# Kernel optimization log

Hardware: AMD Instinct MI355X
Metric: run time of the kernel (lower is better)

## Reference

```python
import jax, jax.numpy as jnp
import numpy as np

B, C, V = 4096, 1000, 8000   # batch, NUM_COMPO, NUM_CHARS
THRESH = 0.8                 # compo_score_thresh
SCALE = 0.1                  # score_adjustment_scale
TOPK = 5


def setup_inputs() -> dict:
    key = jax.random.key(0)
    k1, k2, k3, k4 = jax.random.split(key, 4)
    return {
        "pred_class_logits": jax.random.normal(k1, (B, V), jnp.float32),
        "pred_compo_logits": jax.random.normal(k2, (B, C), jnp.float32),
        "compo_co_occurrence_prob": jax.random.uniform(k3, (C, C), dtype=jnp.float32),
        "compo_chinese_matrix": jax.random.randint(k4, (C, V), 0, 2, dtype=jnp.int32),
    }


def _decode_one(compo_scores, co_occ, matrix):
    """components_to_chinese_char for one sample. compo_scores:[C], co_occ:[C,C], matrix:[C,V]."""
    nC, nV = matrix.shape
    # score adjustment from co-occurrence of components above threshold
    sel = compo_scores > THRESH                                   # [C]
    adj = SCALE * jnp.sum(
        jnp.where(sel[:, None], co_occ * compo_scores[:, None], 0.0), axis=0)  # [C]
    scores = compo_scores + adj
    max_idx = jnp.argmax(scores)
    max_score = scores[max_idx]
    # re-threshold and sort selected scores descending (fixed-shape: mask with -inf)
    sel2 = scores > THRESH
    num_selected = jnp.sum(sel2.astype(jnp.int32))
    masked = jnp.where(sel2, scores, -jnp.inf)
    order = jnp.argsort(-masked)          # descending; selected compo indices first
    sorted_scores = masked[order]
    hit0 = matrix[max_idx]                # [V] 0/1

    def cond(carry):
        i, hit, _ = carry
        return (i < num_selected) & (jnp.sum(hit) > 1)

    def body(carry):
        i, hit, _ = carry
        row = matrix[order[i]]
        new_hit = jnp.where(hit + row == 2, 1, 0).astype(jnp.int32)  # intersection
        return (i + 1, new_hit, hit)

    i0 = jnp.array(1, jnp.int32)
    i, hit, prev = jax.lax.while_loop(cond, body, (i0, hit0, hit0))
    empty = jnp.sum(hit) == 0
    i = jnp.where(empty, i - 1, i)
    hit = jnp.where(empty, prev, hit)
    hit_score = jnp.where(i == 1, max_score, sorted_scores[jnp.maximum(i - 1, 0)])
    # first 5 hit char indices (ascending, as tf.where yields), padded with -1
    char_ids = jnp.where(hit == 1, jnp.arange(nV), nV)
    first5 = jnp.sort(char_ids)[:TOPK]
    hit_indices = jnp.where(first5 == nV, -1, first5).astype(jnp.int32)
    return hit_indices, hit_score


def reference(pred_class_logits, pred_compo_logits, compo_co_occurrence_prob, compo_chinese_matrix):
    class_probs = jax.nn.softmax(pred_class_logits, axis=1)            # [B,V]
    class_scores, class_indices = jax.lax.top_k(class_probs, TOPK)     # [B,5]
    compo_scores = jax.nn.sigmoid(pred_compo_logits)                   # [B,C]
    hit_indices, hit_scores = jax.vmap(_decode_one, in_axes=(0, None, None))(
        compo_scores, compo_co_occurrence_prob, compo_chinese_matrix)
    class_indices = class_indices.astype(jnp.int32)
    num_hit = jnp.sum((hit_indices != -1).astype(jnp.int32), axis=1)   # [B]
    combined1 = jnp.where(num_hit == 1, hit_indices[:, 0], class_indices[:, 0])
    combined2 = jnp.where((class_scores[:, 0] < 0.85) & (num_hit == 1),
                          hit_indices[:, 0], class_indices[:, 0])
    return (class_indices, class_scores, hit_indices, hit_scores, combined1, combined2)
```

## Files before the change

### kernel.cpp

```cpp
#include <hip/hip_runtime.h>
#include <cstdint>
#include <cstddef>

#define B_SZ 4096
#define C_SZ 1000
#define V_SZ 8000
#define RW 128
#define THRESHF 0.8f
#define SCALEF 0.1f

#define OFF_CI 0
#define OFF_CS (B_SZ * 5)
#define OFF_HI (2 * B_SZ * 5)
#define OFF_HS (3 * B_SZ * 5)
#define OFF_C1 (3 * B_SZ * 5 + B_SZ)
#define OFF_C2 (3 * B_SZ * 5 + 2 * B_SZ)

__global__ __launch_bounds__(256) void pack_kernel(const int* __restrict__ mat,
                                                   unsigned long long* __restrict__ packed) {
  const int c = blockIdx.x;
  const int tid = threadIdx.x;
  const int lane = tid & 63;
  const int wv = tid >> 6;
  const int* row = mat + (size_t)c * V_SZ;
  for (int base = 0; base < 8192; base += 256) {
    const int k = base + tid;
    int v = 0;
    if (k < V_SZ) v = row[k];
    unsigned long long msk = __ballot(v != 0);
    if (lane == 0) packed[(size_t)c * RW + ((base >> 6) + wv)] = msk;
  }
}

__global__ __launch_bounds__(256) void class_topk_kernel(const float* __restrict__ logits,
                                                         float* __restrict__ out) {
  const int b = blockIdx.x;
  const int tid = threadIdx.x;
  const int lane = tid & 63;
  const int wv = tid >> 6;
  const float* row = logits + (size_t)b * V_SZ;
  float v[32];
#pragma unroll
  for (int q = 0; q < 32; ++q) {
    int k = tid + (q << 8);
    v[q] = (k < V_SZ) ? row[k] : -INFINITY;
  }
  __shared__ float sred[4];
  __shared__ int sredi[4];
  float lm = -INFINITY;
#pragma unroll
  for (int q = 0; q < 32; ++q) lm = fmaxf(lm, v[q]);
#pragma unroll
  for (int o = 32; o >= 1; o >>= 1) lm = fmaxf(lm, __shfl_xor(lm, o));
  if (lane == 0) sred[wv] = lm;
  __syncthreads();
  const float m = fmaxf(fmaxf(sred[0], sred[1]), fmaxf(sred[2], sred[3]));
  float ls = 0.f;
#pragma unroll
  for (int q = 0; q < 32; ++q) ls += expf(v[q] - m);
#pragma unroll
  for (int o = 32; o >= 1; o >>= 1) ls += __shfl_xor(ls, o);
  __syncthreads();
  if (lane == 0) sred[wv] = ls;
  __syncthreads();
  const float ssum = sred[0] + sred[1] + sred[2] + sred[3];
  for (int r = 0; r < 5; ++r) {
    float bv = -INFINITY;
    int bi = 0;
#pragma unroll
    for (int q = 0; q < 32; ++q) {
      if (v[q] > bv) { bv = v[q]; bi = tid + (q << 8); }
    }
#pragma unroll
    for (int o = 32; o >= 1; o >>= 1) {
      float ov = __shfl_xor(bv, o);
      int oi = __shfl_xor(bi, o);
      if (ov > bv || (ov == bv && oi < bi)) { bv = ov; bi = oi; }
    }
    __syncthreads();
    if (lane == 0) { sred[wv] = bv; sredi[wv] = bi; }
    __syncthreads();
    bv = sred[0]; bi = sredi[0];
#pragma unroll
    for (int w = 1; w < 4; ++w) {
      if (sred[w] > bv || (sred[w] == bv && sredi[w] < bi)) { bv = sred[w]; bi = sredi[w]; }
    }
    if ((bi & 255) == tid) {
      const int sl = bi >> 8;
#pragma unroll
      for (int q = 0; q < 32; ++q)
        if (q == sl) v[q] = -INFINITY;
    }
    if (tid == 0) {
      out[OFF_CI + b * 5 + r] = (float)bi;
      out[OFF_CS + b * 5 + r] = expf(bv - m) / ssum;
    }
  }
}

__global__ __launch_bounds__(256) void decode_kernel(const float* __restrict__ compo_logits,
                                                     const float* __restrict__ co_occ,
                                                     const unsigned long long* __restrict__ packed,
                                                     float* __restrict__ out) {
  const int b = blockIdx.x;
  const int tid = threadIdx.x;
  const int lane = tid & 63;
  const int wv = tid >> 6;
  __shared__ float s_m[C_SZ];
  __shared__ float s_sc[1024];
  __shared__ short s_list[C_SZ];
  __shared__ int s_nsel;
  __shared__ float red_v[4];
  __shared__ int red_i[4];
  __shared__ int red_n[4];

  const float* lg = compo_logits + (size_t)b * C_SZ;
  for (int k = tid; k < 1024; k += 256) {
    if (k < C_SZ) {
      float x = lg[k];
      float s = 1.0f / (1.0f + expf(-x));
      s_sc[k] = s;
      s_m[k] = (s > THRESHF) ? s : 0.0f;
    } else {
      s_sc[k] = -INFINITY;
    }
  }
  __syncthreads();
  if (wv == 0) {
    int off = 0;
    for (int base = 0; base < C_SZ; base += 64) {
      const int k = base + lane;
      float mv = (k < C_SZ) ? s_m[k] : 0.0f;
      unsigned long long msk = __ballot(mv != 0.0f);
      int rank = __popcll(msk & ((1ull << lane) - 1ull));
      if (mv != 0.0f) s_list[off + rank] = (short)k;
      off += __popcll(msk);
    }
    if (lane == 0) s_nsel = off;
  }
  __syncthreads();
  const int nadj = s_nsel;
  float a0 = 0.f, a1 = 0.f, a2 = 0.f, a3 = 0.f;
  for (int e = 0; e < nadj; ++e) {
    const int i = s_list[e];
    const float mm = s_m[i];
    const float* rp = co_occ + (size_t)i * C_SZ;
    a0 += mm * rp[tid];
    a1 += mm * rp[tid + 256];
    a2 += mm * rp[tid + 512];
    if (tid < C_SZ - 768) a3 += mm * rp[tid + 768];
  }
  float bv = -INFINITY;
  int bi = 0;
  int cnt = 0;
  {
    float sc;
    sc = s_sc[tid] + SCALEF * a0;
    s_sc[tid] = sc;
    if (sc > THRESHF) cnt++;
    if (sc > bv) { bv = sc; bi = tid; }
    sc = s_sc[tid + 256] + SCALEF * a1;
    s_sc[tid + 256] = sc;
    if (sc > THRESHF) cnt++;
    if (sc > bv) { bv = sc; bi = tid + 256; }
    sc = s_sc[tid + 512] + SCALEF * a2;
    s_sc[tid + 512] = sc;
    if (sc > THRESHF) cnt++;
    if (sc > bv) { bv = sc; bi = tid + 512; }
    if (tid < C_SZ - 768) {
      sc = s_sc[tid + 768] + SCALEF * a3;
      s_sc[tid + 768] = sc;
      if (sc > THRESHF) cnt++;
      if (sc > bv) { bv = sc; bi = tid + 768; }
    }
  }
#pragma unroll
  for (int o = 32; o >= 1; o >>= 1) {
    float ov = __shfl_xor(bv, o);
    int oi = __shfl_xor(bi, o);
    cnt += __shfl_xor(cnt, o);
    if (ov > bv || (ov == bv && oi < bi)) { bv = ov; bi = oi; }
  }
  if (lane == 0) { red_v[wv] = bv; red_i[wv] = bi; red_n[wv] = cnt; }
  __syncthreads();
  float mxv = red_v[0];
  int mxi = red_i[0];
  const int nsel = red_n[0] + red_n[1] + red_n[2] + red_n[3];
#pragma unroll
  for (int w = 1; w < 4; ++w) {
    if (red_v[w] > mxv || (red_v[w] == mxv && red_i[w] < mxi)) { mxv = red_v[w]; mxi = red_i[w]; }
  }
  if (tid == 0) s_sc[mxi] = -INFINITY;
  __syncthreads();
  if (wv != 0) return;

  float p[16];
#pragma unroll
  for (int q = 0; q < 16; ++q) {
    const int k = lane + (q << 6);
    p[q] = (k < C_SZ) ? s_sc[k] : -INFINITY;
  }
  const unsigned long long* pr = packed + (size_t)mxi * RW;
  unsigned long long h0 = pr[lane];
  unsigned long long h1 = pr[64 + lane];
  int pc = __popcll(h0) + __popcll(h1);
#pragma unroll
  for (int o = 32; o >= 1; o >>= 1) pc += __shfl_xor(pc, o);
  int i = 1;
  float last_v = mxv;
  unsigned long long ph0 = h0, ph1 = h1;
  int ppc = pc;
  float plast = mxv;
  while (i < nsel && pc > 1) {
    float ev = -INFINITY;
    int ei = 0;
#pragma unroll
    for (int q = 0; q < 16; ++q) {
      if (p[q] > ev) { ev = p[q]; ei = lane + (q << 6); }
    }
#pragma unroll
    for (int o = 32; o >= 1; o >>= 1) {
      float ov = __shfl_xor(ev, o);
      int oi = __shfl_xor(ei, o);
      if (ov > ev || (ov == ev && oi < ei)) { ev = ov; ei = oi; }
    }
    if ((ei & 63) == lane) {
      const int sl = ei >> 6;
#pragma unroll
      for (int q = 0; q < 16; ++q)
        if (q == sl) p[q] = -INFINITY;
    }
    const unsigned long long* r2 = packed + (size_t)ei * RW;
    ph0 = h0; ph1 = h1; ppc = pc; plast = last_v;
    h0 &= r2[lane];
    h1 &= r2[64 + lane];
    pc = __popcll(h0) + __popcll(h1);
#pragma unroll
    for (int o = 32; o >= 1; o >>= 1) pc += __shfl_xor(pc, o);
    last_v = ev;
    ++i;
  }
  if (pc == 0) {
    h0 = ph0; h1 = ph1; pc = ppc; last_v = plast;
  }
  const float hit_score = last_v;

  const int c0 = __popcll(h0), c1 = __popcll(h1);
  int s0 = c0;
#pragma unroll
  for (int o = 1; o < 64; o <<= 1) {
    int n = __shfl_up(s0, o);
    if (lane >= o) s0 += n;
  }
  const int tot0 = __shfl(s0, 63);
  const int pre0 = s0 - c0;
  int s1 = c1;
#pragma unroll
  for (int o = 1; o < 64; o <<= 1) {
    int n = __shfl_up(s1, o);
    if (lane >= o) s1 += n;
  }
  const int tot = tot0 + __shfl(s1, 63);
  const int pre1 = tot0 + s1 - c1;
  {
    unsigned long long x = h0;
    int r = pre0;
    while (x && r < 5) {
      int bp = __ffsll((unsigned long long)x) - 1;
      out[OFF_HI + b * 5 + r] = (float)((lane << 6) + bp);
      x &= x - 1;
      ++r;
    }
    x = h1;
    r = pre1;
    while (x && r < 5) {
      int bp = __ffsll((unsigned long long)x) - 1;
      out[OFF_HI + b * 5 + r] = (float)(((64 + lane) << 6) + bp);
      x &= x - 1;
      ++r;
    }
  }
  int fb = 0x7fffffff;
  if (c0) fb = (lane << 6) + __ffsll((unsigned long long)h0) - 1;
  else if (c1) fb = ((64 + lane) << 6) + __ffsll((unsigned long long)h1) - 1;
#pragma unroll
  for (int o = 32; o >= 1; o >>= 1) fb = min(fb, __shfl_xor(fb, o));
  if (lane == 0) {
    const int num_hit = tot < 5 ? tot : 5;
    for (int r = num_hit; r < 5; ++r) out[OFF_HI + b * 5 + r] = -1.0f;
    out[OFF_HS + b] = hit_score;
    const float ci0 = out[OFF_CI + b * 5];
    const float cs0 = out[OFF_CS + b * 5];
    out[OFF_C1 + b] = (num_hit == 1) ? (float)fb : ci0;
    out[OFF_C2 + b] = (cs0 < 0.85f && num_hit == 1) ? (float)fb : ci0;
  }
}

extern "C" void kernel_launch(void* const* d_in, const int* in_sizes, int n_in,
                              void* d_out, int out_size, void* d_ws, size_t ws_size,
                              hipStream_t stream) {
  (void)in_sizes; (void)n_in; (void)out_size; (void)ws_size;
  const float* class_logits = (const float*)d_in[0];
  const float* compo_logits = (const float*)d_in[1];
  const float* co_occ = (const float*)d_in[2];
  const int* mat = (const int*)d_in[3];
  float* out = (float*)d_out;
  unsigned long long* packed = (unsigned long long*)d_ws;

  pack_kernel<<<C_SZ, 256, 0, stream>>>(mat, packed);
  class_topk_kernel<<<B_SZ, 256, 0, stream>>>(class_logits, out);
  decode_kernel<<<B_SZ, 256, 0, stream>>>(compo_logits, co_occ, packed, out);
}
```

Measured before the change: 156.7 us.

## Batch sorted intersection across all four waves with shared-memory row staging

Rewrites the decode kernel's sequential greedy intersection. Before, one wave pulled one next-best component per iteration and did a dependent global load each time. Now all four waves select their local top-16 candidates, a merge step picks a global batch of 16, their packed rows are staged into LDS cooperatively, and running popcounts find the stop point inside the batch. It also switches the co-occurrence adjustment and the sigmoid load to float4 vectorised access, unrolled over four selected rows. The cost is more synchronisation per batch and extra LDS, which can lower occupancy, plus complex tie and stop handling that could diverge from the reference in edge cases.

```diff
diff --git a/kernel.cpp b/kernel.cpp
--- a/kernel.cpp
+++ b/kernel.cpp
@@ -1,6 +1,8 @@
 #include <hip/hip_runtime.h>
 #include <cstdint>
 #include <cstddef>
+
+typedef unsigned long long u64;
 
 #define B_SZ 4096
 #define C_SZ 1000
@@ -17,7 +19,7 @@
 #define OFF_C2 (3 * B_SZ * 5 + 2 * B_SZ)
 
 __global__ __launch_bounds__(256) void pack_kernel(const int* __restrict__ mat,
-                                                   unsigned long long* __restrict__ packed) {
+                                                   u64* __restrict__ packed) {
   const int c = blockIdx.x;
   const int tid = threadIdx.x;
   const int lane = tid & 63;
@@ -27,7 +29,7 @@
     const int k = base + tid;
     int v = 0;
     if (k < V_SZ) v = row[k];
-    unsigned long long msk = __ballot(v != 0);
+    u64 msk = __ballot(v != 0);
     if (lane == 0) packed[(size_t)c * RW + ((base >> 6) + wv)] = msk;
   }
 }
@@ -100,79 +102,102 @@
 
 __global__ __launch_bounds__(256) void decode_kernel(const float* __restrict__ compo_logits,
                                                      const float* __restrict__ co_occ,
-                                                     const unsigned long long* __restrict__ packed,
+                                                     const u64* __restrict__ packed,
                                                      float* __restrict__ out) {
   const int b = blockIdx.x;
   const int tid = threadIdx.x;
   const int lane = tid & 63;
   const int wv = tid >> 6;
-  __shared__ float s_m[C_SZ];
+
   __shared__ float s_sc[1024];
-  __shared__ short s_list[C_SZ];
-  __shared__ int s_nsel;
+  __shared__ int s_list[C_SZ];
+  __shared__ u64 s_rows[16][128];
+  __shared__ float s_wv_v[4][16];
+  __shared__ int s_wv_i[4][16];
+  __shared__ float s_gv[16];
+  __shared__ int s_gi[16];
   __shared__ float red_v[4];
   __shared__ int red_i[4];
   __shared__ int red_n[4];
+  __shared__ int s_nsel2;
+  __shared__ int s_mxi;
+  __shared__ float s_mxv;
+  __shared__ int s_nadj;
+  __shared__ int s_ctl;
 
   const float* lg = compo_logits + (size_t)b * C_SZ;
-  for (int k = tid; k < 1024; k += 256) {
-    if (k < C_SZ) {
-      float x = lg[k];
-      float s = 1.0f / (1.0f + expf(-x));
-      s_sc[k] = s;
-      s_m[k] = (s > THRESHF) ? s : 0.0f;
-    } else {
-      s_sc[k] = -INFINITY;
-    }
-  }
-  __syncthreads();
+  if (tid < 250) {
+    float4 x = ((const float4*)lg)[tid];
+    s_sc[4 * tid + 0] = 1.0f / (1.0f + expf(-x.x));
+    s_sc[4 * tid + 1] = 1.0f / (1.0f + expf(-x.y));
+    s_sc[4 * tid + 2] = 1.0f / (1.0f + expf(-x.z));
+    s_sc[4 * tid + 3] = 1.0f / (1.0f + expf(-x.w));
+  } else {
+    s_sc[4 * tid + 0] = -INFINITY;
+    s_sc[4 * tid + 1] = -INFINITY;
+    s_sc[4 * tid + 2] = -INFINITY;
+    s_sc[4 * tid + 3] = -INFINITY;
+  }
+  __syncthreads();
+
   if (wv == 0) {
     int off = 0;
     for (int base = 0; base < C_SZ; base += 64) {
       const int k = base + lane;
-      float mv = (k < C_SZ) ? s_m[k] : 0.0f;
-      unsigned long long msk = __ballot(mv != 0.0f);
+      float mv = (k < C_SZ) ? s_sc[k] : -INFINITY;
+      bool sel = (k < C_SZ) && (mv > THRESHF);
+      u64 msk = __ballot(sel);
       int rank = __popcll(msk & ((1ull << lane) - 1ull));
-      if (mv != 0.0f) s_list[off + rank] = (short)k;
+      if (sel) s_list[off + rank] = k;
       off += __popcll(msk);
     }
-    if (lane == 0) s_nsel = off;
-  }
-  __syncthreads();
-  const int nadj = s_nsel;
+    if (lane == 0) s_nadj = off;
+  }
+  __syncthreads();
+  const int nadj = s_nadj;
+
   float a0 = 0.f, a1 = 0.f, a2 = 0.f, a3 = 0.f;
-  for (int e = 0; e < nadj; ++e) {
-    const int i = s_list[e];
-    const float mm = s_m[i];
-    const float* rp = co_occ + (size_t)i * C_SZ;
-    a0 += mm * rp[tid];
-    a1 += mm * rp[tid + 256];
-    a2 += mm * rp[tid + 512];
-    if (tid < C_SZ - 768) a3 += mm * rp[tid + 768];
-  }
+  if (tid < 250) {
+    const float4* cov = (const float4*)co_occ;
+    int e = 0;
+    for (; e + 4 <= nadj; e += 4) {
+      int i0 = s_list[e], i1 = s_list[e + 1], i2 = s_list[e + 2], i3 = s_list[e + 3];
+      float m0 = s_sc[i0], m1 = s_sc[i1], m2 = s_sc[i2], m3 = s_sc[i3];
+      float4 v0 = cov[i0 * 250 + tid];
+      float4 v1 = cov[i1 * 250 + tid];
+      float4 v2 = cov[i2 * 250 + tid];
+      float4 v3 = cov[i3 * 250 + tid];
+      a0 += m0 * v0.x; a0 += m1 * v1.x; a0 += m2 * v2.x; a0 += m3 * v3.x;
+      a1 += m0 * v0.y; a1 += m1 * v1.y; a1 += m2 * v2.y; a1 += m3 * v3.y;
+      a2 += m0 * v0.z; a2 += m1 * v1.z; a2 += m2 * v2.z; a2 += m3 * v3.z;
+      a3 += m0 * v0.w; a3 += m1 * v1.w; a3 += m2 * v2.w; a3 += m3 * v3.w;
+    }
+    for (; e < nadj; ++e) {
+      int i = s_list[e];
+      float m = s_sc[i];
+      float4 v = cov[i * 250 + tid];
+      a0 += m * v.x; a1 += m * v.y; a2 += m * v.z; a3 += m * v.w;
+    }
+  }
+  __syncthreads();
+
   float bv = -INFINITY;
   int bi = 0;
   int cnt = 0;
-  {
+  if (tid < 250) {
     float sc;
-    sc = s_sc[tid] + SCALEF * a0;
-    s_sc[tid] = sc;
+    sc = s_sc[4 * tid + 0] + SCALEF * a0; s_sc[4 * tid + 0] = sc;
     if (sc > THRESHF) cnt++;
-    if (sc > bv) { bv = sc; bi = tid; }
-    sc = s_sc[tid + 256] + SCALEF * a1;
-    s_sc[tid + 256] = sc;
+    if (sc > bv) { bv = sc; bi = 4 * tid + 0; }
+    sc = s_sc[4 * tid + 1] + SCALEF * a1; s_sc[4 * tid + 1] = sc;
     if (sc > THRESHF) cnt++;
-    if (sc > bv) { bv = sc; bi = tid + 256; }
-    sc = s_sc[tid + 512] + SCALEF * a2;
-    s_sc[tid + 512] = sc;
+    if (sc > bv) { bv = sc; bi = 4 * tid + 1; }
+    sc = s_sc[4 * tid + 2] + SCALEF * a2; s_sc[4 * tid + 2] = sc;
     if (sc > THRESHF) cnt++;
-    if (sc > bv) { bv = sc; bi = tid + 512; }
-    if (tid < C_SZ - 768) {
-      sc = s_sc[tid + 768] + SCALEF * a3;
-      s_sc[tid + 768] = sc;
-      if (sc > THRESHF) cnt++;
-      if (sc > bv) { bv = sc; bi = tid + 768; }
-    }
+    if (sc > bv) { bv = sc; bi = 4 * tid + 2; }
+    sc = s_sc[4 * tid + 3] + SCALEF * a3; s_sc[4 * tid + 3] = sc;
+    if (sc > THRESHF) cnt++;
+    if (sc > bv) { bv = sc; bi = 4 * tid + 3; }
   }
 #pragma unroll
   for (int o = 32; o >= 1; o >>= 1) {
@@ -183,116 +208,211 @@
   }
   if (lane == 0) { red_v[wv] = bv; red_i[wv] = bi; red_n[wv] = cnt; }
   __syncthreads();
-  float mxv = red_v[0];
-  int mxi = red_i[0];
-  const int nsel = red_n[0] + red_n[1] + red_n[2] + red_n[3];
-#pragma unroll
-  for (int w = 1; w < 4; ++w) {
-    if (red_v[w] > mxv || (red_v[w] == mxv && red_i[w] < mxi)) { mxv = red_v[w]; mxi = red_i[w]; }
-  }
-  if (tid == 0) s_sc[mxi] = -INFINITY;
-  __syncthreads();
-  if (wv != 0) return;
-
-  float p[16];
-#pragma unroll
-  for (int q = 0; q < 16; ++q) {
-    const int k = lane + (q << 6);
-    p[q] = (k < C_SZ) ? s_sc[k] : -INFINITY;
-  }
-  const unsigned long long* pr = packed + (size_t)mxi * RW;
-  unsigned long long h0 = pr[lane];
-  unsigned long long h1 = pr[64 + lane];
-  int pc = __popcll(h0) + __popcll(h1);
-#pragma unroll
-  for (int o = 32; o >= 1; o >>= 1) pc += __shfl_xor(pc, o);
-  int i = 1;
-  float last_v = mxv;
-  unsigned long long ph0 = h0, ph1 = h1;
-  int ppc = pc;
-  float plast = mxv;
-  while (i < nsel && pc > 1) {
-    float ev = -INFINITY;
-    int ei = 0;
-#pragma unroll
-    for (int q = 0; q < 16; ++q) {
-      if (p[q] > ev) { ev = p[q]; ei = lane + (q << 6); }
-    }
-#pragma unroll
-    for (int o = 32; o >= 1; o >>= 1) {
-      float ov = __shfl_xor(ev, o);
-      int oi = __shfl_xor(ei, o);
-      if (ov > ev || (ov == ev && oi < ei)) { ev = ov; ei = oi; }
-    }
-    if ((ei & 63) == lane) {
-      const int sl = ei >> 6;
-#pragma unroll
-      for (int q = 0; q < 16; ++q)
-        if (q == sl) p[q] = -INFINITY;
-    }
-    const unsigned long long* r2 = packed + (size_t)ei * RW;
-    ph0 = h0; ph1 = h1; ppc = pc; plast = last_v;
-    h0 &= r2[lane];
-    h1 &= r2[64 + lane];
-    pc = __popcll(h0) + __popcll(h1);
-#pragma unroll
-    for (int o = 32; o >= 1; o >>= 1) pc += __shfl_xor(pc, o);
-    last_v = ev;
-    ++i;
-  }
-  if (pc == 0) {
-    h0 = ph0; h1 = ph1; pc = ppc; last_v = plast;
-  }
-  const float hit_score = last_v;
-
-  const int c0 = __popcll(h0), c1 = __popcll(h1);
-  int s0 = c0;
-#pragma unroll
-  for (int o = 1; o < 64; o <<= 1) {
-    int n = __shfl_up(s0, o);
-    if (lane >= o) s0 += n;
-  }
-  const int tot0 = __shfl(s0, 63);
-  const int pre0 = s0 - c0;
-  int s1 = c1;
-#pragma unroll
-  for (int o = 1; o < 64; o <<= 1) {
-    int n = __shfl_up(s1, o);
-    if (lane >= o) s1 += n;
-  }
-  const int tot = tot0 + __shfl(s1, 63);
-  const int pre1 = tot0 + s1 - c1;
-  {
-    unsigned long long x = h0;
-    int r = pre0;
-    while (x && r < 5) {
-      int bp = __ffsll((unsigned long long)x) - 1;
-      out[OFF_HI + b * 5 + r] = (float)((lane << 6) + bp);
-      x &= x - 1;
-      ++r;
-    }
-    x = h1;
-    r = pre1;
-    while (x && r < 5) {
-      int bp = __ffsll((unsigned long long)x) - 1;
-      out[OFF_HI + b * 5 + r] = (float)(((64 + lane) << 6) + bp);
-      x &= x - 1;
-      ++r;
-    }
-  }
-  int fb = 0x7fffffff;
-  if (c0) fb = (lane << 6) + __ffsll((unsigned long long)h0) - 1;
-  else if (c1) fb = ((64 + lane) << 6) + __ffsll((unsigned long long)h1) - 1;
-#pragma unroll
-  for (int o = 32; o >= 1; o >>= 1) fb = min(fb, __shfl_xor(fb, o));
-  if (lane == 0) {
-    const int num_hit = tot < 5 ? tot : 5;
-    for (int r = num_hit; r < 5; ++r) out[OFF_HI + b * 5 + r] = -1.0f;
-    out[OFF_HS + b] = hit_score;
-    const float ci0 = out[OFF_CI + b * 5];
-    const float cs0 = out[OFF_CS + b * 5];
-    out[OFF_C1 + b] = (num_hit == 1) ? (float)fb : ci0;
-    out[OFF_C2 + b] = (cs0 < 0.85f && num_hit == 1) ? (float)fb : ci0;
+  if (tid == 0) {
+    float mv = red_v[0];
+    int mi = red_i[0];
+    for (int w = 1; w < 4; ++w)
+      if (red_v[w] > mv || (red_v[w] == mv && red_i[w] < mi)) { mv = red_v[w]; mi = red_i[w]; }
+    s_mxv = mv; s_mxi = mi;
+    s_nsel2 = red_n[0] + red_n[1] + red_n[2] + red_n[3];
+  }
+  __syncthreads();
+  const float mxv = s_mxv;
+  const int mxi = s_mxi;
+  const int nsel = s_nsel2;
+
+  const int ebase = wv << 8;
+  float r0 = s_sc[ebase + lane];
+  float r1 = s_sc[ebase + lane + 64];
+  float r2 = s_sc[ebase + lane + 128];
+  float r3 = s_sc[ebase + lane + 192];
+
+  u64 acc0 = ~0ull, acc1 = ~0ull;
+  float prev_last = mxv;
+  float hitscore = mxv;
+
+  for (int batch = 0; batch < 64; ++batch) {
+    {
+      int rd = 0;
+      for (; rd < 16; ++rd) {
+        float ev = r0;
+        int ei = ebase + lane;
+        if (r1 > ev) { ev = r1; ei = ebase + lane + 64; }
+        if (r2 > ev) { ev = r2; ei = ebase + lane + 128; }
+        if (r3 > ev) { ev = r3; ei = ebase + lane + 192; }
+#pragma unroll
+        for (int o = 32; o >= 1; o >>= 1) {
+          float ov = __shfl_xor(ev, o);
+          int oi = __shfl_xor(ei, o);
+          if (ov > ev || (ov == ev && oi < ei)) { ev = ov; ei = oi; }
+        }
+        if (!(ev > THRESHF)) break;
+        if (lane == 0) { s_wv_v[wv][rd] = ev; s_wv_i[wv][rd] = ei; }
+        int d = ei - ebase;
+        if ((d & 63) == lane) {
+          if (d < 64) r0 = -INFINITY;
+          else if (d < 128) r1 = -INFINITY;
+          else if (d < 192) r2 = -INFINITY;
+          else r3 = -INFINITY;
+        }
+      }
+      if (lane == 0)
+        for (; rd < 16; ++rd) s_wv_v[wv][rd] = -INFINITY;
+    }
+    __syncthreads();
+    if (wv == 0) {
+      float cv = s_wv_v[lane >> 4][lane & 15];
+      int ci = s_wv_i[lane >> 4][lane & 15];
+      int rd = 0;
+      for (; rd < 16; ++rd) {
+        float ev = cv;
+        int ei = ci;
+#pragma unroll
+        for (int o = 32; o >= 1; o >>= 1) {
+          float ov = __shfl_xor(ev, o);
+          int oi = __shfl_xor(ei, o);
+          if (ov > ev || (ov == ev && oi < ei)) { ev = ov; ei = oi; }
+        }
+        if (!(ev > THRESHF)) break;
+        if (lane == 0) { s_gi[rd] = ei; s_gv[rd] = ev; }
+        if (ci == ei) cv = -INFINITY;
+      }
+      if (lane == 0) {
+        for (; rd < 16; ++rd) s_gi[rd] = -1;
+        if (nsel == 0 && batch == 0) { s_gi[0] = mxi; s_gv[0] = mxv; }
+      }
+    }
+    __syncthreads();
+    for (int j = 0; j < 16; ++j) {
+      float val = s_wv_v[wv][j];
+      if (val == -INFINITY) break;
+      int idx = s_wv_i[wv][j];
+      bool consumed = false;
+#pragma unroll
+      for (int k = 0; k < 16; ++k) consumed |= (s_gi[k] == idx);
+      if (!consumed) {
+        int d = idx - ebase;
+        if ((d & 63) == lane) {
+          if (d < 64) r0 = val;
+          else if (d < 128) r1 = val;
+          else if (d < 192) r2 = val;
+          else r3 = val;
+        }
+      }
+    }
+    {
+      int k = tid >> 4;
+      int g = s_gi[k];
+      if (g >= 0) {
+        const u64* src = packed + (size_t)g * RW + ((tid & 15) << 3);
+        u64* dst = &s_rows[k][(tid & 15) << 3];
+#pragma unroll
+        for (int w = 0; w < 8; ++w) dst[w] = src[w];
+      }
+    }
+    __syncthreads();
+    if (wv == 0) {
+      u64 bal = __ballot(lane < 16 && s_gi[lane] >= 0);
+      int take = __popcll(bal);
+      u64 na0 = acc0, na1 = acc1;
+      u64 pk0 = 0, pk1 = 0, pk2 = 0, pk3 = 0;
+      for (int k = 0; k < take; ++k) {
+        na0 &= s_rows[k][lane];
+        na1 &= s_rows[k][64 + lane];
+        u64 pc = (u64)(__popcll(na0) + __popcll(na1));
+        int sh = (k & 3) << 4;
+        if (k < 4) pk0 |= pc << sh;
+        else if (k < 8) pk1 |= pc << sh;
+        else if (k < 12) pk2 |= pc << sh;
+        else pk3 |= pc << sh;
+      }
+#pragma unroll
+      for (int o = 32; o >= 1; o >>= 1) {
+        pk0 += __shfl_xor(pk0, o);
+        pk1 += __shfl_xor(pk1, o);
+        pk2 += __shfl_xor(pk2, o);
+        pk3 += __shfl_xor(pk3, o);
+      }
+      int kstar = -1;
+      unsigned pcs = 0;
+      for (int k = 0; k < take; ++k) {
+        int sh = (k & 3) << 4;
+        u64 w = (k < 4) ? pk0 : ((k < 8) ? pk1 : ((k < 12) ? pk2 : pk3));
+        unsigned pcv = (unsigned)((w >> sh) & 0xffffull);
+        if (pcv <= 1u) { kstar = k; pcs = pcv; break; }
+      }
+      int stop, kfin;
+      if (take == 0) { stop = 1; kfin = 0; hitscore = prev_last; }
+      else if (kstar >= 0) {
+        if (pcs == 0) {
+          stop = 1;
+          if (kstar == 0) { kfin = 0; hitscore = prev_last; }
+          else { kfin = kstar; hitscore = s_gv[kstar - 1]; }
+        } else { stop = 1; kfin = kstar + 1; hitscore = s_gv[kstar]; }
+      } else if (take < 16) { stop = 1; kfin = take; hitscore = s_gv[take - 1]; }
+      else { stop = 0; kfin = 16; }
+      for (int k = 0; k < kfin; ++k) {
+        acc0 &= s_rows[k][lane];
+        acc1 &= s_rows[k][64 + lane];
+      }
+      if (!stop) prev_last = s_gv[15];
+      if (lane == 0) s_ctl = stop;
+    }
+    __syncthreads();
+    if (s_ctl) break;
+  }
+
+  if (wv == 0) {
+    u64 h0 = acc0, h1 = acc1;
+    const int c0 = __popcll(h0), c1 = __popcll(h1);
+    int sc0 = c0;
+#pragma unroll
+    for (int o = 1; o < 64; o <<= 1) {
+      int n = __shfl_up(sc0, o);
+      if (lane >= o) sc0 += n;
+    }
+    const int tot0 = __shfl(sc0, 63);
+    const int pre0 = sc0 - c0;
+    int sc1 = c1;
+#pragma unroll
+    for (int o = 1; o < 64; o <<= 1) {
+      int n = __shfl_up(sc1, o);
+      if (lane >= o) sc1 += n;
+    }
+    const int tot = tot0 + __shfl(sc1, 63);
+    const int pre1 = tot0 + sc1 - c1;
+    {
+      u64 x = h0;
+      int r = pre0;
+      while (x && r < 5) {
+        int bp = __ffsll((unsigned long long)x) - 1;
+        out[OFF_HI + b * 5 + r] = (float)((lane << 6) + bp);
+        x &= x - 1;
+        ++r;
+      }
+      x = h1;
+      r = pre1;
+      while (x && r < 5) {
+        int bp = __ffsll((unsigned long long)x) - 1;
+        out[OFF_HI + b * 5 + r] = (float)(((64 + lane) << 6) + bp);
+        x &= x - 1;
+        ++r;
+      }
+    }
+    int fb = 0x7fffffff;
+    if (c0) fb = (lane << 6) + __ffsll((unsigned long long)h0) - 1;
+    else if (c1) fb = ((64 + lane) << 6) + __ffsll((unsigned long long)h1) - 1;
+#pragma unroll
+    for (int o = 32; o >= 1; o >>= 1) fb = min(fb, __shfl_xor(fb, o));
+    if (lane == 0) {
+      const int num_hit = tot < 5 ? tot : 5;
+      for (int r = num_hit; r < 5; ++r) out[OFF_HI + b * 5 + r] = -1.0f;
+      out[OFF_HS + b] = hitscore;
+      const float ci0 = out[OFF_CI + b * 5];
+      const float cs0 = out[OFF_CS + b * 5];
+      out[OFF_C1 + b] = (num_hit == 1) ? (float)fb : ci0;
+      out[OFF_C2 + b] = (cs0 < 0.85f && num_hit == 1) ? (float)fb : ci0;
+    }
   }
 }
 
@@ -305,7 +425,7 @@
   const float* co_occ = (const float*)d_in[2];
   const int* mat = (const int*)d_in[3];
   float* out = (float*)d_out;
-  unsigned long long* packed = (unsigned long long*)d_ws;
+  u64* packed = (u64*)d_ws;
 
   pack_kernel<<<C_SZ, 256, 0, stream>>>(mat, packed);
   class_topk_kernel<<<B_SZ, 256, 0, stream>>>(class_logits, out);
```

Result: slower. 246.3 us (+57.1%).

## Split decode into batched co-occurrence matvec and wave-per-sample speculative intersection tail

Applied to the files above, without the earlier changes.

Replaces the per-sample decode kernel with two kernels. The first computes the co-occurrence score adjustment for 8 samples per block, so each co_occ row loaded with float4 is shared across samples, and writes the adjusted scores to workspace. The second runs one wavefront per sample, using packed 64-bit value/index keys and intersecting up to 8 candidate rows speculatively per step to shorten the serial while loop. The class top-k load is also vectorized to float4, at the cost of an extra workspace round trip and a fourth launch.

```diff
diff --git a/kernel.cpp b/kernel.cpp
--- a/kernel.cpp
+++ b/kernel.cpp
@@ -1,6 +1,8 @@
 #include <hip/hip_runtime.h>
 #include <cstdint>
 #include <cstddef>
+
+typedef unsigned long long u64;
 
 #define B_SZ 4096
 #define C_SZ 1000
@@ -8,6 +10,7 @@
 #define RW 128
 #define THRESHF 0.8f
 #define SCALEF 0.1f
+#define S_MV 8
 
 #define OFF_CI 0
 #define OFF_CS (B_SZ * 5)
@@ -17,7 +20,7 @@
 #define OFF_C2 (3 * B_SZ * 5 + 2 * B_SZ)
 
 __global__ __launch_bounds__(256) void pack_kernel(const int* __restrict__ mat,
-                                                   unsigned long long* __restrict__ packed) {
+                                                   u64* __restrict__ packed) {
   const int c = blockIdx.x;
   const int tid = threadIdx.x;
   const int lane = tid & 63;
@@ -27,7 +30,7 @@
     const int k = base + tid;
     int v = 0;
     if (k < V_SZ) v = row[k];
-    unsigned long long msk = __ballot(v != 0);
+    u64 msk = __ballot(v != 0);
     if (lane == 0) packed[(size_t)c * RW + ((base >> 6) + wv)] = msk;
   }
 }
@@ -41,9 +44,15 @@
   const float* row = logits + (size_t)b * V_SZ;
   float v[32];
 #pragma unroll
-  for (int q = 0; q < 32; ++q) {
-    int k = tid + (q << 8);
-    v[q] = (k < V_SZ) ? row[k] : -INFINITY;
+  for (int f = 0; f < 8; ++f) {
+    const int base = (f << 10) + (tid << 2);
+    if (base < V_SZ) {
+      float4 x = *(const float4*)(row + base);
+      v[4 * f + 0] = x.x; v[4 * f + 1] = x.y; v[4 * f + 2] = x.z; v[4 * f + 3] = x.w;
+    } else {
+      v[4 * f + 0] = -INFINITY; v[4 * f + 1] = -INFINITY;
+      v[4 * f + 2] = -INFINITY; v[4 * f + 3] = -INFINITY;
+    }
   }
   __shared__ float sred[4];
   __shared__ int sredi[4];
@@ -69,7 +78,8 @@
     int bi = 0;
 #pragma unroll
     for (int q = 0; q < 32; ++q) {
-      if (v[q] > bv) { bv = v[q]; bi = tid + (q << 8); }
+      const int idx = ((q >> 2) << 10) + (tid << 2) + (q & 3);
+      if (v[q] > bv) { bv = v[q]; bi = idx; }
     }
 #pragma unroll
     for (int o = 32; o >= 1; o >>= 1) {
@@ -85,8 +95,8 @@
     for (int w = 1; w < 4; ++w) {
       if (sred[w] > bv || (sred[w] == bv && sredi[w] < bi)) { bv = sred[w]; bi = sredi[w]; }
     }
-    if ((bi & 255) == tid) {
-      const int sl = bi >> 8;
+    if (((bi & 1023) >> 2) == tid) {
+      const int sl = ((bi >> 10) << 2) | (bi & 3);
 #pragma unroll
       for (int q = 0; q < 32; ++q)
         if (q == sl) v[q] = -INFINITY;
@@ -98,175 +108,218 @@
   }
 }
 
-__global__ __launch_bounds__(256) void decode_kernel(const float* __restrict__ compo_logits,
+__global__ __launch_bounds__(256) void matvec_kernel(const float* __restrict__ compo_logits,
                                                      const float* __restrict__ co_occ,
-                                                     const unsigned long long* __restrict__ packed,
-                                                     float* __restrict__ out) {
-  const int b = blockIdx.x;
+                                                     float* __restrict__ sc_arr) {
+  const int b0 = blockIdx.x * S_MV;
   const int tid = threadIdx.x;
   const int lane = tid & 63;
-  const int wv = tid >> 6;
-  __shared__ float s_m[C_SZ];
-  __shared__ float s_sc[1024];
-  __shared__ short s_list[C_SZ];
-  __shared__ int s_nsel;
-  __shared__ float red_v[4];
-  __shared__ int red_i[4];
-  __shared__ int red_n[4];
-
-  const float* lg = compo_logits + (size_t)b * C_SZ;
-  for (int k = tid; k < 1024; k += 256) {
-    if (k < C_SZ) {
-      float x = lg[k];
-      float s = 1.0f / (1.0f + expf(-x));
-      s_sc[k] = s;
-      s_m[k] = (s > THRESHF) ? s : 0.0f;
-    } else {
-      s_sc[k] = -INFINITY;
-    }
-  }
-  __syncthreads();
-  if (wv == 0) {
-    int off = 0;
-    for (int base = 0; base < C_SZ; base += 64) {
-      const int k = base + lane;
-      float mv = (k < C_SZ) ? s_m[k] : 0.0f;
-      unsigned long long msk = __ballot(mv != 0.0f);
-      int rank = __popcll(msk & ((1ull << lane) - 1ull));
-      if (mv != 0.0f) s_list[off + rank] = (short)k;
-      off += __popcll(msk);
-    }
-    if (lane == 0) s_nsel = off;
-  }
-  __syncthreads();
-  const int nadj = s_nsel;
-  float a0 = 0.f, a1 = 0.f, a2 = 0.f, a3 = 0.f;
-  for (int e = 0; e < nadj; ++e) {
-    const int i = s_list[e];
-    const float mm = s_m[i];
-    const float* rp = co_occ + (size_t)i * C_SZ;
-    a0 += mm * rp[tid];
-    a1 += mm * rp[tid + 256];
-    a2 += mm * rp[tid + 512];
-    if (tid < C_SZ - 768) a3 += mm * rp[tid + 768];
-  }
-  float bv = -INFINITY;
-  int bi = 0;
+  const int w = tid >> 6;
+  __shared__ float s_sc[S_MV][C_SZ];
+  __shared__ unsigned s_bm[C_SZ];
+
+  for (int idx = tid; idx < S_MV * 250; idx += 256) {
+    const int sp = idx / 250;
+    const int f = idx - sp * 250;
+    float4 x = ((const float4*)(compo_logits + (size_t)(b0 + sp) * C_SZ))[f];
+    s_sc[sp][4 * f + 0] = 1.0f / (1.0f + expf(-x.x));
+    s_sc[sp][4 * f + 1] = 1.0f / (1.0f + expf(-x.y));
+    s_sc[sp][4 * f + 2] = 1.0f / (1.0f + expf(-x.z));
+    s_sc[sp][4 * f + 3] = 1.0f / (1.0f + expf(-x.w));
+  }
+  __syncthreads();
+  for (int i = tid; i < C_SZ; i += 256) {
+    unsigned mk = 0;
+#pragma unroll
+    for (int sp = 0; sp < S_MV; ++sp) mk |= (s_sc[sp][i] > THRESHF ? 1u : 0u) << sp;
+    s_bm[i] = mk;
+  }
+  __syncthreads();
+  float acc[2][16];
+#pragma unroll
+  for (int s = 0; s < 2; ++s)
+#pragma unroll
+    for (int j = 0; j < 16; ++j) acc[s][j] = 0.0f;
+  const int cb = lane << 4;
+  const unsigned wsel = 0x11u << w;
+  for (int i = 0; i < C_SZ; ++i) {
+    const unsigned bmv = s_bm[i];
+    if (!(bmv & wsel)) continue;
+    float cv[16];
+#pragma unroll
+    for (int f = 0; f < 4; ++f) {
+      const int base = cb + 4 * f;
+      if (base < C_SZ) {
+        float4 x = *(const float4*)(co_occ + (size_t)i * C_SZ + base);
+        cv[4 * f + 0] = x.x; cv[4 * f + 1] = x.y; cv[4 * f + 2] = x.z; cv[4 * f + 3] = x.w;
+      } else {
+        cv[4 * f + 0] = 0.f; cv[4 * f + 1] = 0.f; cv[4 * f + 2] = 0.f; cv[4 * f + 3] = 0.f;
+      }
+    }
+#pragma unroll
+    for (int spl = 0; spl < 2; ++spl) {
+      const int sp = w + 4 * spl;
+      if (bmv & (1u << sp)) {
+        const float ms = s_sc[sp][i];
+#pragma unroll
+        for (int j = 0; j < 16; ++j) acc[spl][j] += ms * cv[j];
+      }
+    }
+  }
+#pragma unroll
+  for (int spl = 0; spl < 2; ++spl) {
+    const int sp = w + 4 * spl;
+    float* dst = sc_arr + (size_t)(b0 + sp) * C_SZ;
+#pragma unroll
+    for (int f = 0; f < 4; ++f) {
+      const int base = cb + 4 * f;
+      if (base < C_SZ) {
+        float4 o;
+        o.x = s_sc[sp][base + 0] + SCALEF * acc[spl][4 * f + 0];
+        o.y = s_sc[sp][base + 1] + SCALEF * acc[spl][4 * f + 1];
+        o.z = s_sc[sp][base + 2] + SCALEF * acc[spl][4 * f + 2];
+        o.w = s_sc[sp][base + 3] + SCALEF * acc[spl][4 * f + 3];
+        *(float4*)(dst + base) = o;
+      }
+    }
+  }
+}
+
+__global__ __launch_bounds__(256) void tail_kernel(const float* __restrict__ sc_arr,
+                                                   const u64* __restrict__ packed,
+                                                   float* __restrict__ out) {
+  const int b = blockIdx.x * 4 + (threadIdx.x >> 6);
+  const int lane = threadIdx.x & 63;
+  const float* sc = sc_arr + (size_t)b * C_SZ;
+  u64 key[16];
+  unsigned avail = 0;
   int cnt = 0;
-  {
-    float sc;
-    sc = s_sc[tid] + SCALEF * a0;
-    s_sc[tid] = sc;
-    if (sc > THRESHF) cnt++;
-    if (sc > bv) { bv = sc; bi = tid; }
-    sc = s_sc[tid + 256] + SCALEF * a1;
-    s_sc[tid + 256] = sc;
-    if (sc > THRESHF) cnt++;
-    if (sc > bv) { bv = sc; bi = tid + 256; }
-    sc = s_sc[tid + 512] + SCALEF * a2;
-    s_sc[tid + 512] = sc;
-    if (sc > THRESHF) cnt++;
-    if (sc > bv) { bv = sc; bi = tid + 512; }
-    if (tid < C_SZ - 768) {
-      sc = s_sc[tid + 768] + SCALEF * a3;
-      s_sc[tid + 768] = sc;
-      if (sc > THRESHF) cnt++;
-      if (sc > bv) { bv = sc; bi = tid + 768; }
-    }
-  }
-#pragma unroll
-  for (int o = 32; o >= 1; o >>= 1) {
-    float ov = __shfl_xor(bv, o);
-    int oi = __shfl_xor(bi, o);
-    cnt += __shfl_xor(cnt, o);
-    if (ov > bv || (ov == bv && oi < bi)) { bv = ov; bi = oi; }
-  }
-  if (lane == 0) { red_v[wv] = bv; red_i[wv] = bi; red_n[wv] = cnt; }
-  __syncthreads();
-  float mxv = red_v[0];
-  int mxi = red_i[0];
-  const int nsel = red_n[0] + red_n[1] + red_n[2] + red_n[3];
-#pragma unroll
-  for (int w = 1; w < 4; ++w) {
-    if (red_v[w] > mxv || (red_v[w] == mxv && red_i[w] < mxi)) { mxv = red_v[w]; mxi = red_i[w]; }
-  }
-  if (tid == 0) s_sc[mxi] = -INFINITY;
-  __syncthreads();
-  if (wv != 0) return;
-
-  float p[16];
+  u64 kb = 0;
 #pragma unroll
   for (int q = 0; q < 16; ++q) {
-    const int k = lane + (q << 6);
-    p[q] = (k < C_SZ) ? s_sc[k] : -INFINITY;
-  }
-  const unsigned long long* pr = packed + (size_t)mxi * RW;
-  unsigned long long h0 = pr[lane];
-  unsigned long long h1 = pr[64 + lane];
+    const int col = lane + (q << 6);
+    if (col < C_SZ) {
+      const float s = sc[col];
+      const u64 k = ((u64)__float_as_uint(s) << 32) | (u64)(0xFFFFFFFFu - (unsigned)col);
+      key[q] = k;
+      if (k > kb) kb = k;
+      if (s > THRESHF) { avail |= 1u << q; cnt++; }
+    } else key[q] = 0;
+  }
+  u64 mk = kb;
+#pragma unroll
+  for (int o = 32; o >= 1; o >>= 1) { u64 t = __shfl_xor(mk, o); if (t > mk) mk = t; }
+  const float mxv = __uint_as_float((unsigned)(mk >> 32));
+  const int mxi = (int)(0xFFFFFFFFu - (unsigned)(mk & 0xFFFFFFFFull));
+#pragma unroll
+  for (int o = 32; o >= 1; o >>= 1) cnt += __shfl_xor(cnt, o);
+  const int nsel = cnt;
+  if ((mxi & 63) == lane) avail &= ~(1u << (mxi >> 6));
+  const u64* pr = packed + (size_t)mxi * RW;
+  u64 h0 = pr[lane], h1 = pr[64 + lane];
   int pc = __popcll(h0) + __popcll(h1);
 #pragma unroll
   for (int o = 32; o >= 1; o >>= 1) pc += __shfl_xor(pc, o);
   int i = 1;
-  float last_v = mxv;
-  unsigned long long ph0 = h0, ph1 = h1;
-  int ppc = pc;
-  float plast = mxv;
-  while (i < nsel && pc > 1) {
-    float ev = -INFINITY;
-    int ei = 0;
-#pragma unroll
-    for (int q = 0; q < 16; ++q) {
-      if (p[q] > ev) { ev = p[q]; ei = lane + (q << 6); }
-    }
-#pragma unroll
-    for (int o = 32; o >= 1; o >>= 1) {
-      float ov = __shfl_xor(ev, o);
-      int oi = __shfl_xor(ei, o);
-      if (ov > ev || (ov == ev && oi < ei)) { ev = ov; ei = oi; }
-    }
-    if ((ei & 63) == lane) {
-      const int sl = ei >> 6;
-#pragma unroll
-      for (int q = 0; q < 16; ++q)
-        if (q == sl) p[q] = -INFINITY;
-    }
-    const unsigned long long* r2 = packed + (size_t)ei * RW;
-    ph0 = h0; ph1 = h1; ppc = pc; plast = last_v;
-    h0 &= r2[lane];
-    h1 &= r2[64 + lane];
-    pc = __popcll(h0) + __popcll(h1);
-#pragma unroll
-    for (int o = 32; o >= 1; o >>= 1) pc += __shfl_xor(pc, o);
-    last_v = ev;
-    ++i;
-  }
-  if (pc == 0) {
-    h0 = ph0; h1 = ph1; pc = ppc; last_v = plast;
-  }
-  const float hit_score = last_v;
-
-  const int c0 = __popcll(h0), c1 = __popcll(h1);
-  int s0 = c0;
+  float last_val = mxv;
+  if (nsel >= 2 && pc > 1) {
+    for (;;) {
+      int kt = (nsel - i < 8) ? (nsel - i) : 8;
+      float cval[8];
+      int cidx[8];
+      u64 rl[8], rh[8];
+      float lastc = last_val;
+      int kv = 0;
+#pragma unroll
+      for (int k = 0; k < 8; ++k) {
+        cval[k] = 0.0f; cidx[k] = -1;
+        if (k < kt) {
+          u64 lm = 0;
+#pragma unroll
+          for (int q = 0; q < 16; ++q)
+            if (avail & (1u << q)) { if (key[q] > lm) lm = key[q]; }
+          u64 ck = lm;
+#pragma unroll
+          for (int o = 32; o >= 1; o >>= 1) { u64 t = __shfl_xor(ck, o); if (t > ck) ck = t; }
+          if (ck != 0) {
+            cval[k] = __uint_as_float((unsigned)(ck >> 32));
+            cidx[k] = (int)(0xFFFFFFFFu - (unsigned)(ck & 0xFFFFFFFFull));
+            if ((cidx[k] & 63) == lane) avail &= ~(1u << (cidx[k] >> 6));
+            lastc = cval[k];
+            kv = k + 1;
+          }
+        }
+      }
+      kt = kv;
+      if (kt == 0) break;
+#pragma unroll
+      for (int k = 0; k < 8; ++k) {
+        if (k < kt) {
+          const u64* rp = packed + (size_t)cidx[k] * RW;
+          rl[k] = rp[lane]; rh[k] = rp[64 + lane];
+        } else { rl[k] = ~0ull; rh[k] = ~0ull; }
+      }
+      u64 c0 = h0, c1 = h1, pk0 = 0, pk1 = 0;
+#pragma unroll
+      for (int k = 0; k < 8; ++k) {
+        c0 &= rl[k]; c1 &= rh[k];
+        const u64 p = (u64)(__popcll(c0) + __popcll(c1));
+        if (k < 4) pk0 |= p << (k * 16); else pk1 |= p << ((k - 4) * 16);
+      }
+#pragma unroll
+      for (int o = 32; o >= 1; o >>= 1) { pk0 += __shfl_xor(pk0, o); pk1 += __shfl_xor(pk1, o); }
+      int kstar = -1;
+      unsigned pcv = 0;
+#pragma unroll
+      for (int k = 0; k < 8; ++k) {
+        if (k < kt && kstar < 0) {
+          const unsigned f = (unsigned)(((k < 4 ? pk0 : pk1) >> ((k & 3) * 16)) & 0xFFFFull);
+          if (f <= 1u) { kstar = k; pcv = f; }
+        }
+      }
+      if (kstar >= 0) {
+        float vk = 0.f, vkm1 = last_val;
+#pragma unroll
+        for (int k = 0; k < 8; ++k)
+          if (k == kstar) { vk = cval[k]; if (k > 0) vkm1 = cval[k - 1]; }
+        const int na = (pcv == 1u) ? (kstar + 1) : kstar;
+#pragma unroll
+        for (int k = 0; k < 8; ++k) if (k < na) { h0 &= rl[k]; h1 &= rh[k]; }
+        if (pcv == 1u) { i += kstar + 1; last_val = vk; }
+        else { i += kstar; last_val = vkm1; }
+        break;
+      }
+#pragma unroll
+      for (int k = 0; k < 8; ++k) if (k < kt) { h0 &= rl[k]; h1 &= rh[k]; }
+      i += kt;
+      last_val = lastc;
+      if (i >= nsel) break;
+    }
+  }
+  const float hit_score = (i == 1) ? mxv : last_val;
+
+  const int c0n = __popcll(h0), c1n = __popcll(h1);
+  int s0 = c0n;
 #pragma unroll
   for (int o = 1; o < 64; o <<= 1) {
     int n = __shfl_up(s0, o);
     if (lane >= o) s0 += n;
   }
   const int tot0 = __shfl(s0, 63);
-  const int pre0 = s0 - c0;
-  int s1 = c1;
+  const int pre0 = s0 - c0n;
+  int s1 = c1n;
 #pragma unroll
   for (int o = 1; o < 64; o <<= 1) {
     int n = __shfl_up(s1, o);
     if (lane >= o) s1 += n;
   }
   const int tot = tot0 + __shfl(s1, 63);
-  const int pre1 = tot0 + s1 - c1;
+  const int pre1 = tot0 + s1 - c1n;
   {
-    unsigned long long x = h0;
+    u64 x = h0;
     int r = pre0;
     while (x && r < 5) {
-      int bp = __ffsll((unsigned long long)x) - 1;
+      const int bp = __ffsll((unsigned long long)x) - 1;
       out[OFF_HI + b * 5 + r] = (float)((lane << 6) + bp);
       x &= x - 1;
       ++r;
@@ -274,15 +327,15 @@
     x = h1;
     r = pre1;
     while (x && r < 5) {
-      int bp = __ffsll((unsigned long long)x) - 1;
+      const int bp = __ffsll((unsigned long long)x) - 1;
       out[OFF_HI + b * 5 + r] = (float)(((64 + lane) << 6) + bp);
       x &= x - 1;
       ++r;
     }
   }
   int fb = 0x7fffffff;
-  if (c0) fb = (lane << 6) + __ffsll((unsigned long long)h0) - 1;
-  else if (c1) fb = ((64 + lane) << 6) + __ffsll((unsigned long long)h1) - 1;
+  if (c0n) fb = (lane << 6) + __ffsll((unsigned long long)h0) - 1;
+  else if (c1n) fb = ((64 + lane) << 6) + __ffsll((unsigned long long)h1) - 1;
 #pragma unroll
   for (int o = 32; o >= 1; o >>= 1) fb = min(fb, __shfl_xor(fb, o));
   if (lane == 0) {
@@ -305,9 +358,11 @@
   const float* co_occ = (const float*)d_in[2];
   const int* mat = (const int*)d_in[3];
   float* out = (float*)d_out;
-  unsigned long long* packed = (unsigned long long*)d_ws;
+  u64* packed = (u64*)d_ws;
+  float* sc_arr = (float*)((char*)d_ws + (size_t)C_SZ * RW * 8);
 
   pack_kernel<<<C_SZ, 256, 0, stream>>>(mat, packed);
   class_topk_kernel<<<B_SZ, 256, 0, stream>>>(class_logits, out);
-  decode_kernel<<<B_SZ, 256, 0, stream>>>(compo_logits, co_occ, packed, out);
-}
+  matvec_kernel<<<B_SZ / S_MV, 256, 0, stream>>>(compo_logits, co_occ, sc_arr);
+  tail_kernel<<<B_SZ / 4, 256, 0, stream>>>(sc_arr, packed, out);
+}
```

Result: slower. 222.9 us (+42.3%).
